# Kernel tuning notes

Measured on AMD Instinct MI355X. Metric: run time of the kernel, lower is better.

## Reference

```python
import jax, jax.numpy as jnp
import numpy as np

S = 14
B = 2
C = 20
LAMBDA_COORD = 5.0
LAMBDA_NOOBJ = 0.5
BATCH = 4096


def setup_inputs() -> dict:
    key = jax.random.key(0)
    k1, k2, k3 = jax.random.split(key, 3)
    pred = jax.random.uniform(k1, (BATCH, S, S, B * 5 + C), dtype=jnp.float32)
    target = jax.random.uniform(k2, (BATCH, S, S, B * 5 + C), dtype=jnp.float32)
    obj = (jax.random.uniform(k3, (BATCH, S, S), dtype=jnp.float32) < 0.15).astype(jnp.float32)
    target = target.at[..., 4].set(obj)
    target = target.at[..., 9].set(obj)
    return {"pred": pred, "target": target}


def _iou(box1, box2):
    # box1, box2: (..., 4) = [x, y, w, h]; elementwise IoU over leading dims
    b1x1 = box1[..., 0] - box1[..., 2] / 2
    b1y1 = box1[..., 1] - box1[..., 3] / 2
    b1x2 = box1[..., 0] + box1[..., 2] / 2
    b1y2 = box1[..., 1] + box1[..., 3] / 2
    b2x1 = box2[..., 0] - box2[..., 2] / 2
    b2y1 = box2[..., 1] - box2[..., 3] / 2
    b2x2 = box2[..., 0] + box2[..., 2] / 2
    b2y2 = box2[..., 1] + box2[..., 3] / 2
    iw = jnp.clip(jnp.minimum(b1x2, b2x2) - jnp.maximum(b1x1, b2x1), 0)
    ih = jnp.clip(jnp.minimum(b1y2, b2y2) - jnp.maximum(b1y1, b2y1), 0)
    inter = iw * ih
    a1 = (b1x2 - b1x1) * (b1y2 - b1y1)
    a2 = (b2x2 - b2x1) * (b2y2 - b2y1)
    return inter / (a1 + a2 - inter + 1e-6)


def reference(pred, target):
    bs = pred.shape[0]
    tb = target[..., : B * 5].reshape(bs, S, S, B, 5)
    pb = pred[..., : B * 5].reshape(bs, S, S, B, 5)
    tcls = target[..., B * 5 :]
    pcls = pred[..., B * 5 :]

    obj_mask = tb[..., 4] > 0          # (bs,S,S,B)
    has_obj = obj_mask[..., 0]         # (bs,S,S)
    noobj_mask = ~obj_mask

    # no-object confidence loss over every non-obj box slot
    conf_err2 = (pb[..., 4] - tb[..., 4]) ** 2
    noobj_loss = jnp.sum(jnp.where(noobj_mask, conf_err2, 0.0))

    # per-box IoU between i-th pred box and i-th target box in each cell
    ious = _iou(pb[..., :4], tb[..., :4])            # (bs,S,S,B)
    best_idx = jnp.argmax(ious, axis=-1)             # (bs,S,S)
    idx = best_idx[..., None, None]
    p_best = jnp.take_along_axis(pb, idx, axis=3)[..., 0, :]  # (bs,S,S,5)
    t_best = jnp.take_along_axis(tb, idx, axis=3)[..., 0, :]

    m = has_obj                                       # (bs,S,S) bool
    mf = m.astype(pred.dtype)

    xy_loss = jnp.sum(mf[..., None] * (p_best[..., :2] - t_best[..., :2]) ** 2)
    p_wh = jnp.sqrt(jnp.abs(p_best[..., 2:4]) + 1e-6)
    t_wh_safe = jnp.where(m[..., None], t_best[..., 2:4], 1.0)  # avoid sqrt(0) grad NaN
    t_wh = jnp.sqrt(t_wh_safe)
    wh_loss = jnp.sum(mf[..., None] * (p_wh - t_wh) ** 2)
    coord_loss = xy_loss + wh_loss

    obj_loss = jnp.sum(mf * (p_best[..., 4] - t_best[..., 4]) ** 2)

    # non-best box confidence pushed to 0 (B=2: the other slot)
    nonbest_conf = jnp.sum(pb[..., 4], axis=-1) - p_best[..., 4]
    noobj_loss = noobj_loss + LAMBDA_NOOBJ * jnp.sum(mf * nonbest_conf ** 2)

    class_loss = jnp.sum(mf[..., None] * (pcls - tcls) ** 2)

    total = LAMBDA_COORD * coord_loss + obj_loss + LAMBDA_NOOBJ * noobj_loss + class_loss
    return total / bs
```

## Files before the change

kernel.cpp:

```cpp
#include <hip/hip_runtime.h>


#define FEAT 30
#define CELLS 802816
#define TILE_CELLS 64
#define TILE_FLOATS (TILE_CELLS * FEAT)
#define NB (CELLS / TILE_CELLS)
#define RED_TPB 256

__device__ __forceinline__ void load16(const float* g, float* l) {
    __builtin_amdgcn_global_load_lds(
        (const __attribute__((address_space(1))) void*)g,
        (__attribute__((address_space(3))) void*)l, 16, 0, 0);
}

__device__ __forceinline__ float iou_f(float x1, float y1, float w1, float h1,
                                       float x2, float y2, float w2, float h2) {
    float b1x1 = x1 - 0.5f * w1, b1x2 = x1 + 0.5f * w1;
    float b1y1 = y1 - 0.5f * h1, b1y2 = y1 + 0.5f * h1;
    float b2x1 = x2 - 0.5f * w2, b2x2 = x2 + 0.5f * w2;
    float b2y1 = y2 - 0.5f * h2, b2y2 = y2 + 0.5f * h2;
    float iw = fmaxf(fminf(b1x2, b2x2) - fmaxf(b1x1, b2x1), 0.0f);
    float ih = fmaxf(fminf(b1y2, b2y2) - fmaxf(b1y1, b2y1), 0.0f);
    float inter = iw * ih;
    float a1 = (b1x2 - b1x1) * (b1y2 - b1y1);
    float a2 = (b2x2 - b2x1) * (b2y2 - b2y1);
    return inter / (a1 + a2 - inter + 1e-6f);
}

__device__ __forceinline__ float cell_loss(const float* p, const float* t) {
    const bool obj0 = t[4] > 0.0f;
    const bool obj1 = t[9] > 0.0f;
    const float mf = obj0 ? 1.0f : 0.0f;

    float d0 = p[4] - t[4];
    float d1 = p[9] - t[9];
    float noobj = (obj0 ? 0.0f : d0 * d0) + (obj1 ? 0.0f : d1 * d1);

    float iou0 = iou_f(p[0], p[1], p[2], p[3], t[0], t[1], t[2], t[3]);
    float iou1 = iou_f(p[5], p[6], p[7], p[8], t[5], t[6], t[7], t[8]);
    const bool sel1 = iou1 > iou0;

    float pbx = sel1 ? p[5] : p[0];
    float pby = sel1 ? p[6] : p[1];
    float pbw = sel1 ? p[7] : p[2];
    float pbh = sel1 ? p[8] : p[3];
    float pbc = sel1 ? p[9] : p[4];
    float tbx = sel1 ? t[5] : t[0];
    float tby = sel1 ? t[6] : t[1];
    float tbw = sel1 ? t[7] : t[2];
    float tbh = sel1 ? t[8] : t[3];
    float tbc = sel1 ? t[9] : t[4];

    float dx = pbx - tbx, dy = pby - tby;
    float xy = dx * dx + dy * dy;

    float pw = sqrtf(fabsf(pbw) + 1e-6f);
    float ph = sqrtf(fabsf(pbh) + 1e-6f);
    float tw = sqrtf(obj0 ? tbw : 1.0f);
    float th = sqrtf(obj0 ? tbh : 1.0f);
    float dw = pw - tw, dh = ph - th;
    float wh = dw * dw + dh * dh;

    float dc = pbc - tbc;
    float obj_l = dc * dc;

    float nonbest = (p[4] + p[9]) - pbc;
    noobj += 0.5f * mf * nonbest * nonbest;

    float cls = 0.0f;
#pragma unroll
    for (int k = 10; k < FEAT; ++k) {
        float d = p[k] - t[k];
        cls += d * d;
    }

    return 5.0f * mf * (xy + wh) + mf * obj_l + 0.5f * noobj + mf * cls;
}

__global__ __launch_bounds__(64) void yolo_kernel(
        const float* __restrict__ pred, const float* __restrict__ tgt,
        float* __restrict__ partials) {
    __shared__ float lds[2 * TILE_FLOATS];

    const int lane = threadIdx.x;
    const float* predT = pred + (long long)blockIdx.x * TILE_FLOATS;
    const float* tgtT  = tgt  + (long long)blockIdx.x * TILE_FLOATS;

    const float* pl = predT + lane * 4;
    const float* ml = (lane < 32) ? (predT + 1792 + lane * 4)
                                  : (tgtT - 128 + lane * 4);
    const float* tl = tgtT + 128 + lane * 4;
#pragma unroll
    for (int j = 0; j < 7; ++j) load16(pl + j * 256, lds + j * 256);
    load16(ml, lds + 1792);
#pragma unroll
    for (int j = 0; j < 7; ++j) load16(tl + j * 256, lds + 2048 + j * 256);

    __builtin_amdgcn_s_waitcnt(0x3f70);

    const float2* pc = (const float2*)(lds + lane * FEAT);
    const float2* tc = (const float2*)(lds + TILE_FLOATS + lane * FEAT);
    float pf[FEAT], tf[FEAT];
#pragma unroll
    for (int k = 0; k < FEAT / 2; ++k) {
        float2 a = pc[k]; pf[2 * k] = a.x; pf[2 * k + 1] = a.y;
        float2 b = tc[k]; tf[2 * k] = b.x; tf[2 * k + 1] = b.y;
    }

    float v = cell_loss(pf, tf);
#pragma unroll
    for (int off = 32; off > 0; off >>= 1) v += __shfl_down(v, off, 64);
    if (lane == 0) partials[blockIdx.x] = v;
}

__global__ __launch_bounds__(RED_TPB) void yolo_reduce_kernel(
        const float* __restrict__ partials, float* __restrict__ out) {
    __shared__ float wave_sum[RED_TPB / 64];
    const int tid = threadIdx.x;
    float v = 0.0f;
#pragma unroll 1
    for (int i = tid; i < NB; i += RED_TPB) v += partials[i];
#pragma unroll
    for (int off = 32; off > 0; off >>= 1) v += __shfl_down(v, off, 64);
    if ((tid & 63) == 0) wave_sum[tid >> 6] = v;
    __syncthreads();
    if (tid == 0)
        out[0] = (wave_sum[0] + wave_sum[1] + wave_sum[2] + wave_sum[3]) *
                 (1.0f / 4096.0f);
}

extern "C" void kernel_launch(void* const* d_in, const int* in_sizes, int n_in,
                              void* d_out, int out_size, void* d_ws, size_t ws_size,
                              hipStream_t stream) {
    const float* pred = (const float*)d_in[0];
    const float* tgt  = (const float*)d_in[1];
    float* out = (float*)d_out;
    float* partials = (float*)d_ws;

    yolo_kernel<<<NB, 64, 0, stream>>>(pred, tgt, partials);
    yolo_reduce_kernel<<<1, RED_TPB, 0, stream>>>(partials, out);
}
```

Baseline: 212.9 us.

## Use persistent grid-stride blocks with register prefetch of the next tile

The kernel now launches a fixed grid of 2560 single-wave blocks instead of one block per 64-cell tile. Each block loops over tiles with a grid stride and double-buffers through registers: the current tile goes into LDS, and the global loads for the next tile are issued before the loss computation. Async global-to-LDS loads are replaced by plain float4 loads plus LDS stores. This targets block launch overhead and exposed memory latency, at the cost of more registers and an extra LDS store pass.

```diff
diff --git a/kernel.cpp b/kernel.cpp
--- a/kernel.cpp
+++ b/kernel.cpp
@@ -5,14 +5,9 @@
 #define CELLS 802816
 #define TILE_CELLS 64
 #define TILE_FLOATS (TILE_CELLS * FEAT)
-#define NB (CELLS / TILE_CELLS)
+#define NTILES (CELLS / TILE_CELLS)
+#define GRID 2560
 #define RED_TPB 256
-
-__device__ __forceinline__ void load16(const float* g, float* l) {
-    __builtin_amdgcn_global_load_lds(
-        (const __attribute__((address_space(1))) void*)g,
-        (__attribute__((address_space(3))) void*)l, 16, 0, 0);
-}
 
 __device__ __forceinline__ float iou_f(float x1, float y1, float w1, float h1,
                                        float x2, float y2, float w2, float h2) {
@@ -78,37 +73,54 @@
     return 5.0f * mf * (xy + wh) + mf * obj_l + 0.5f * noobj + mf * cls;
 }
 
+__device__ __forceinline__ void prefetch(const float* __restrict__ pred,
+                                         const float* __restrict__ tgt,
+                                         long long tile, int lane,
+                                         float4 r[15]) {
+    const float* pb = pred + tile * TILE_FLOATS;
+    const float* tb = tgt + tile * TILE_FLOATS;
+#pragma unroll
+    for (int j = 0; j < 15; ++j) {
+        int g = j * 64 + lane;
+        const float* src = (g < 480) ? (pb + 4 * g) : (tb + 4 * (g - 480));
+        r[j] = *(const float4*)src;
+    }
+}
+
 __global__ __launch_bounds__(64) void yolo_kernel(
         const float* __restrict__ pred, const float* __restrict__ tgt,
         float* __restrict__ partials) {
     __shared__ float lds[2 * TILE_FLOATS];
 
     const int lane = threadIdx.x;
-    const float* predT = pred + (long long)blockIdx.x * TILE_FLOATS;
-    const float* tgtT  = tgt  + (long long)blockIdx.x * TILE_FLOATS;
+    float acc = 0.0f;
 
-    const float* pl = predT + lane * 4;
-    const float* ml = (lane < 32) ? (predT + 1792 + lane * 4)
-                                  : (tgtT - 128 + lane * 4);
-    const float* tl = tgtT + 128 + lane * 4;
+    long long t = blockIdx.x;
+    float4 r[15];
+    prefetch(pred, tgt, t, lane, r);
+
+#pragma unroll 1
+    for (; t < NTILES; ) {
+        float4* L = (float4*)lds;
 #pragma unroll
-    for (int j = 0; j < 7; ++j) load16(pl + j * 256, lds + j * 256);
-    load16(ml, lds + 1792);
+        for (int j = 0; j < 15; ++j) L[j * 64 + lane] = r[j];
+
+        long long nt = t + GRID;
+        prefetch(pred, tgt, (nt < NTILES) ? nt : t, lane, r);
+
+        const float2* pc = (const float2*)(lds + lane * FEAT);
+        const float2* tc = (const float2*)(lds + TILE_FLOATS + lane * FEAT);
+        float pf[FEAT], tf[FEAT];
 #pragma unroll
-    for (int j = 0; j < 7; ++j) load16(tl + j * 256, lds + 2048 + j * 256);
-
-    __builtin_amdgcn_s_waitcnt(0x3f70);
-
-    const float2* pc = (const float2*)(lds + lane * FEAT);
-    const float2* tc = (const float2*)(lds + TILE_FLOATS + lane * FEAT);
-    float pf[FEAT], tf[FEAT];
-#pragma unroll
-    for (int k = 0; k < FEAT / 2; ++k) {
-        float2 a = pc[k]; pf[2 * k] = a.x; pf[2 * k + 1] = a.y;
-        float2 b = tc[k]; tf[2 * k] = b.x; tf[2 * k + 1] = b.y;
+        for (int k = 0; k < FEAT / 2; ++k) {
+            float2 a = pc[k]; pf[2 * k] = a.x; pf[2 * k + 1] = a.y;
+            float2 b = tc[k]; tf[2 * k] = b.x; tf[2 * k + 1] = b.y;
+        }
+        acc += cell_loss(pf, tf);
+        t = nt;
     }
 
-    float v = cell_loss(pf, tf);
+    float v = acc;
 #pragma unroll
     for (int off = 32; off > 0; off >>= 1) v += __shfl_down(v, off, 64);
     if (lane == 0) partials[blockIdx.x] = v;
@@ -120,7 +132,7 @@
     const int tid = threadIdx.x;
     float v = 0.0f;
 #pragma unroll 1
-    for (int i = tid; i < NB; i += RED_TPB) v += partials[i];
+    for (int i = tid; i < GRID; i += RED_TPB) v += partials[i];
 #pragma unroll
     for (int off = 32; off > 0; off >>= 1) v += __shfl_down(v, off, 64);
     if ((tid & 63) == 0) wave_sum[tid >> 6] = v;
@@ -138,6 +150,6 @@
     float* out = (float*)d_out;
     float* partials = (float*)d_ws;
 
-    yolo_kernel<<<NB, 64, 0, stream>>>(pred, tgt, partials);
+    yolo_kernel<<<GRID, 64, 0, stream>>>(pred, tgt, partials);
     yolo_reduce_kernel<<<1, RED_TPB, 0, stream>>>(partials, out);
 }
```

New measurement: 242.2 us. 1.14x slower.
